# Kernel tuning notes

Measured on AMD Instinct MI355X. Metric: run time of the kernel, lower is better.

## Reference

```python
import jax, jax.numpy as jnp
import numpy as np

N = 100000
E = 1600000
IN = 256
H = 4
C = 64


def setup_inputs() -> dict:
    key = jax.random.key(0)
    k1, k2, k3, k4, k5, k6 = jax.random.split(key, 6)
    x = jax.random.normal(k1, (N, IN), dtype=jnp.float32)
    edge_index = jax.random.randint(k2, (2, E), 0, N, dtype=jnp.int64)
    W = jax.random.normal(k3, (IN, H * C), dtype=jnp.float32) * (1.0 / np.sqrt(IN))
    att_src = jax.random.normal(k4, (H, C), dtype=jnp.float32) * 0.1
    att_dst = jax.random.normal(k5, (H, C), dtype=jnp.float32) * 0.1
    bias = jax.random.normal(k6, (H * C,), dtype=jnp.float32) * 0.01
    return {"x": x, "edge_index": edge_index, "W": W, "att_src": att_src, "att_dst": att_dst, "bias": bias}


def reference(x, edge_index, W, att_src, att_dst, bias):
    n = x.shape[0]
    # PyG GATConv default: add self-loops
    loops = jnp.arange(n, dtype=edge_index.dtype)
    src = jnp.concatenate([edge_index[0], loops])  # [E+N]
    dst = jnp.concatenate([edge_index[1], loops])  # [E+N]
    xp = (x @ W).reshape(n, H, C)                   # [N,H,C]
    a_src = jnp.einsum('nhc,hc->nh', xp, att_src)   # [N,H]
    a_dst = jnp.einsum('nhc,hc->nh', xp, att_dst)   # [N,H]
    # per-edge attention logits, LeakyReLU(0.2)
    alpha = jax.nn.leaky_relu(a_src[src] + a_dst[dst], negative_slope=0.2)  # [E+N,H]
    # segment softmax over destination neighborhoods (every node has a self-loop)
    amax = jax.ops.segment_max(alpha, dst, num_segments=n)
    amax = jnp.where(jnp.isfinite(amax), amax, 0.0)
    ex = jnp.exp(alpha - amax[dst])
    denom = jax.ops.segment_sum(ex, dst, num_segments=n)
    w = ex / denom[dst]                              # [E+N,H]
    # weighted scatter-add of source features
    msg = xp[src] * w[..., None]                     # [E+N,H,C]
    agg = jax.ops.segment_sum(msg, dst, num_segments=n)  # [N,H,C]
    out = agg.reshape(n, H * C) + bias
    return jax.nn.elu(out)
```

## Files before the change

### kernel.cpp

```cpp
#include <hip/hip_runtime.h>
#include <hip/hip_fp16.h>

#define FDIM 256
#define NH 4

typedef float f32x4 __attribute__((ext_vector_type(4)));
typedef int   i32x4 __attribute__((ext_vector_type(4)));
typedef short short8v __attribute__((ext_vector_type(8)));
typedef unsigned short ushort_t;
typedef unsigned short ushort8 __attribute__((ext_vector_type(8)));

__device__ __forceinline__ float leaky02(float v) { return v > 0.0f ? v : 0.2f * v; }

__device__ __forceinline__ ushort_t f2bf(float f) {
    union { float f; unsigned int u; } v; v.f = f;
    unsigned int u = v.u + 0x7FFFu + ((v.u >> 16) & 1u);
    return (ushort_t)(u >> 16);
}

__device__ __forceinline__ float bf2f(ushort_t u) {
    union { float f; unsigned int u; } v;
    v.u = ((unsigned int)u) << 16;
    return v.f;
}

__device__ __forceinline__ void gload_lds16(const void* g, void* lds) {
    __builtin_amdgcn_global_load_lds((const __attribute__((address_space(1))) unsigned int*)g,
                                     (__attribute__((address_space(3))) unsigned int*)lds, 16, 0, 0);
}

__device__ __forceinline__ float recw(const i32x4& r, int h) {
    unsigned v = (h < 2) ? (unsigned)r.y : (unsigned)r.z;
    unsigned bits = (h & 1) ? (v >> 16) : (v & 0xFFFFu);
    __half_raw hr; hr.x = (unsigned short)bits;
    return __half2float(*reinterpret_cast<__half*>(&hr));
}

__global__ __launch_bounds__(256) void wprep_kernel(const float* __restrict__ W,
                                                    ushort_t* __restrict__ Wbf) {
    const int k = blockIdx.x;
    const int col = threadIdx.x;
    Wbf[(((size_t)(k >> 3) * 256 + col) << 3) + (k & 7)] = f2bf(W[(size_t)k * 256 + col]);
}

__global__ __launch_bounds__(512) void gemm_xp_kernel(const float* __restrict__ x,
                                                      const ushort_t* __restrict__ Wbf,
                                                      const float* __restrict__ att_s,
                                                      const float* __restrict__ att_d,
                                                      ushort_t* __restrict__ xpb,
                                                      float* __restrict__ a_src,
                                                      float* __restrict__ a_dst, int n,
                                                      const int* __restrict__ dst,
                                                      int* __restrict__ counts, int E) {
    __shared__ ushort_t a_lds[4096];
    __shared__ ushort_t b_lds[8192];
    const int t = threadIdx.x;

    {
        const int per = (E + gridDim.x - 1) / gridDim.x;
        const int lo = blockIdx.x * per;
        const int hi = min(lo + per, E);
        for (int e = lo + t; e < hi; e += 512)
            atomicAdd(&counts[__builtin_nontemporal_load(&dst[e])], 1);
    }

    const int w = t >> 6, l = t & 63;
    const int wm = w >> 2, wn = w & 3;
    const int row0 = blockIdx.x << 7;
    const int fr = l & 15, fk = l >> 4;

    const int arow = t & 127, akb = t >> 7;
    int grow = row0 + arow;
    if (grow >= n) grow = n - 1;
    const float* aptr = x + (size_t)grow * FDIM + (akb << 3);

    f32x4 acc[4][4] = {};

    for (int s = 0; s < 8; ++s) {
        float4 v0 = *(const float4*)(aptr + s * 32);
        float4 v1 = *(const float4*)(aptr + s * 32 + 4);
        ushort8 u;
        u[0]=f2bf(v0.x); u[1]=f2bf(v0.y); u[2]=f2bf(v0.z); u[3]=f2bf(v0.w);
        u[4]=f2bf(v1.x); u[5]=f2bf(v1.y); u[6]=f2bf(v1.z); u[7]=f2bf(v1.w);

        if (s) __syncthreads();

        *(ushort8*)&a_lds[(((size_t)akb << 7) + arow) << 3] = u;
        gload_lds16(Wbf + (size_t)s * 8192 + ((size_t)t << 3), (char*)b_lds + (w << 10));
        gload_lds16(Wbf + (size_t)s * 8192 + ((size_t)(t + 512) << 3), (char*)b_lds + 8192 + (w << 10));
        __syncthreads();

        short8v af[4], bfv[4];
        #pragma unroll
        for (int m = 0; m < 4; ++m)
            af[m] = *(const short8v*)&a_lds[(((size_t)fk << 7) + wm * 64 + m * 16 + fr) << 3];
        #pragma unroll
        for (int nf = 0; nf < 4; ++nf)
            bfv[nf] = *(const short8v*)&b_lds[(((size_t)fk << 8) + wn * 64 + nf * 16 + fr) << 3];
        #pragma unroll
        for (int m = 0; m < 4; ++m)
            #pragma unroll
            for (int nf = 0; nf < 4; ++nf)
                acc[m][nf] = __builtin_amdgcn_mfma_f32_16x16x32_bf16(af[m], bfv[nf], acc[m][nf], 0, 0, 0);
    }

    #pragma unroll
    for (int m = 0; m < 4; ++m) {
        const int r_ = row0 + wm * 64 + m * 16 + fk * 4;
        #pragma unroll
        for (int nf = 0; nf < 4; ++nf) {
            const int c_ = wn * 64 + nf * 16 + fr;
            #pragma unroll
            for (int j = 0; j < 4; ++j)
                if (r_ + j < n)
                    xpb[(size_t)(r_ + j) * FDIM + c_] = f2bf(acc[m][nf][j]);
        }
    }

    float att_sv[4], att_dv[4];
    #pragma unroll
    for (int nf = 0; nf < 4; ++nf) {
        att_sv[nf] = att_s[(wn << 6) + (nf << 4) + fr];
        att_dv[nf] = att_d[(wn << 6) + (nf << 4) + fr];
    }
    #pragma unroll
    for (int m = 0; m < 4; ++m) {
        #pragma unroll
        for (int j = 0; j < 4; ++j) {
            float ps = acc[m][0][j] * att_sv[0] + acc[m][1][j] * att_sv[1]
                     + acc[m][2][j] * att_sv[2] + acc[m][3][j] * att_sv[3];
            float pd = acc[m][0][j] * att_dv[0] + acc[m][1][j] * att_dv[1]
                     + acc[m][2][j] * att_dv[2] + acc[m][3][j] * att_dv[3];
            ps += __shfl_xor(ps, 1, 64); pd += __shfl_xor(pd, 1, 64);
            ps += __shfl_xor(ps, 2, 64); pd += __shfl_xor(pd, 2, 64);
            ps += __shfl_xor(ps, 4, 64); pd += __shfl_xor(pd, 4, 64);
            ps += __shfl_xor(ps, 8, 64); pd += __shfl_xor(pd, 8, 64);
            if (fr == 0) {
                const int r_ = row0 + wm * 64 + m * 16 + fk * 4 + j;
                if (r_ < n) {
                    a_src[r_ * NH + wn] = ps;
                    a_dst[r_ * NH + wn] = pd;
                }
            }
        }
    }
}

__global__ __launch_bounds__(256) void scan_partial_kernel(const int* __restrict__ counts,
                                                           int* __restrict__ blockSums, int n) {
    __shared__ int sdata[256];
    const int b = blockIdx.x, t = threadIdx.x;
    const int base = b * 1024 + t * 4;
    int s = 0;
    #pragma unroll
    for (int j = 0; j < 4; ++j)
        if (base + j < n) s += counts[base + j];
    sdata[t] = s;
    __syncthreads();
    for (int off = 128; off > 0; off >>= 1) {
        if (t < off) sdata[t] += sdata[t + off];
        __syncthreads();
    }
    if (t == 0) blockSums[b] = sdata[0];
}

__global__ __launch_bounds__(256) void scan_final_kernel(const int* __restrict__ counts,
                                                         const int* __restrict__ blockSums,
                                                         int* __restrict__ offsets,
                                                         int* __restrict__ cursor, int n, int nb) {
    __shared__ int s[256];
    __shared__ int bs[256];
    const int b = blockIdx.x, t = threadIdx.x;
    int bv = (t < nb) ? blockSums[t] : 0;
    bs[t] = bv;
    __syncthreads();
    for (int d = 1; d < 256; d <<= 1) {
        int u = (t >= d) ? bs[t - d] : 0;
        __syncthreads();
        bs[t] += u;
        __syncthreads();
    }
    const int blockOff = (b > 0) ? bs[b - 1] : 0;

    const int base = b * 1024 + t * 4;
    int c[4];
    int tsum = 0;
    #pragma unroll
    for (int j = 0; j < 4; ++j) {
        c[j] = (base + j < n) ? counts[base + j] : 0;
        tsum += c[j];
    }
    s[t] = tsum;
    __syncthreads();
    for (int d = 1; d < 256; d <<= 1) {
        int u = (t >= d) ? s[t - d] : 0;
        __syncthreads();
        s[t] += u;
        __syncthreads();
    }
    int run = s[t] - tsum + blockOff;
    #pragma unroll
    for (int j = 0; j < 4; ++j) {
        if (base + j < n) {
            offsets[base + j] = run;
            cursor[base + j] = run;
            run += c[j];
        }
    }
}

__global__ void scatter_kernel(const int* __restrict__ src, const int* __restrict__ dst,
                               const float* __restrict__ a_src, const float* __restrict__ a_dst,
                               int* __restrict__ cursor, i32x4* __restrict__ erec, int E) {
    int stride = gridDim.x * blockDim.x;
    for (int e = blockIdx.x * blockDim.x + threadIdx.x; e < E; e += stride) {
        const int s = __builtin_nontemporal_load(&src[e]);
        const int d = __builtin_nontemporal_load(&dst[e]);
        const float4 as = ((const float4*)a_src)[s];
        const float4 ad = ((const float4*)a_dst)[d];
        const float w0 = __expf(leaky02(as.x + ad.x));
        const float w1 = __expf(leaky02(as.y + ad.y));
        const float w2 = __expf(leaky02(as.z + ad.z));
        const float w3 = __expf(leaky02(as.w + ad.w));
        union { __half2 h; int i; } p01, p23;
        p01.h = __floats2half2_rn(w0, w1);
        p23.h = __floats2half2_rn(w2, w3);
        i32x4 rec;
        rec.x = s; rec.y = p01.i; rec.z = p23.i; rec.w = 0;
        const int pos = atomicAdd(&cursor[d], 1);
        __builtin_nontemporal_store(rec, &erec[pos]);
    }
}

__global__ __launch_bounds__(256) void aggregate_kernel(const ushort_t* __restrict__ xpb,
                                                        const float* __restrict__ a_src,
                                                        const float* __restrict__ a_dst,
                                                        const int* __restrict__ offsets,
                                                        const int* __restrict__ counts,
                                                        const i32x4* __restrict__ erec,
                                                        const float* __restrict__ bias,
                                                        float* __restrict__ out, int n) {
    const int i = (blockIdx.x << 2) + (threadIdx.x >> 6);
    if (i >= n) return;
    const int lane = threadIdx.x & 63;
    const int halfid = lane >> 5, sl = lane & 31;
    const int h = sl >> 3;
    const size_t colb = (size_t)sl << 3;
    const int start = offsets[i];
    const int cnt = counts[i];
    const i32x4* recs = erec + start;

    float acc[8] = {};
    float den = 0.f;

    int e = 0;
    for (; e + 8 <= cnt; e += 8) {
        const i32x4* rp = recs + e + (halfid << 2);
        const i32x4 r0 = rp[0];
        const i32x4 r1 = rp[1];
        const i32x4 r2 = rp[2];
        const i32x4 r3 = rp[3];
        const ushort8 u0 = *(const ushort8*)(xpb + (size_t)r0.x * FDIM + colb);
        const ushort8 u1 = *(const ushort8*)(xpb + (size_t)r1.x * FDIM + colb);
        const ushort8 u2 = *(const ushort8*)(xpb + (size_t)r2.x * FDIM + colb);
        const ushort8 u3 = *(const ushort8*)(xpb + (size_t)r3.x * FDIM + colb);
        const float w0 = recw(r0, h), w1 = recw(r1, h), w2 = recw(r2, h), w3 = recw(r3, h);
        den += (w0 + w1) + (w2 + w3);
        #pragma unroll
        for (int j = 0; j < 8; ++j) acc[j] = fmaf(w0, bf2f(u0[j]), acc[j]);
        #pragma unroll
        for (int j = 0; j < 8; ++j) acc[j] = fmaf(w1, bf2f(u1[j]), acc[j]);
        #pragma unroll
        for (int j = 0; j < 8; ++j) acc[j] = fmaf(w2, bf2f(u2[j]), acc[j]);
        #pragma unroll
        for (int j = 0; j < 8; ++j) acc[j] = fmaf(w3, bf2f(u3[j]), acc[j]);
    }
    for (; e + 2 <= cnt; e += 2) {
        const i32x4 r = recs[e + halfid];
        const ushort8 u = *(const ushort8*)(xpb + (size_t)r.x * FDIM + colb);
        const float wv = recw(r, h);
        den += wv;
        #pragma unroll
        for (int j = 0; j < 8; ++j) acc[j] = fmaf(wv, bf2f(u[j]), acc[j]);
    }
    {
        int srcidx;
        float wv;
        if (halfid == 0) {
            srcidx = i;
            wv = __expf(leaky02(a_src[i * NH + h] + a_dst[i * NH + h]));
        } else if (e < cnt) {
            const i32x4 r = recs[e];
            srcidx = r.x;
            wv = recw(r, h);
        } else {
            srcidx = i;
            wv = 0.f;
        }
        const ushort8 u = *(const ushort8*)(xpb + (size_t)srcidx * FDIM + colb);
        den += wv;
        #pragma unroll
        for (int j = 0; j < 8; ++j) acc[j] = fmaf(wv, bf2f(u[j]), acc[j]);
    }
    den += __shfl_xor(den, 32, 64);
    #pragma unroll
    for (int j = 0; j < 8; ++j) acc[j] += __shfl_xor(acc[j], 32, 64);

    const float inv = 1.0f / den;
    const int c0 = (sl << 3) + (halfid << 2);
    const float4 b4 = *(const float4*)(bias + c0);
    const int jb = halfid << 2;
    f32x4 v;
    v.x = acc[jb + 0] * inv + b4.x;
    v.y = acc[jb + 1] * inv + b4.y;
    v.z = acc[jb + 2] * inv + b4.z;
    v.w = acc[jb + 3] * inv + b4.w;
    v.x = v.x > 0.f ? v.x : (__expf(v.x) - 1.f);
    v.y = v.y > 0.f ? v.y : (__expf(v.y) - 1.f);
    v.z = v.z > 0.f ? v.z : (__expf(v.z) - 1.f);
    v.w = v.w > 0.f ? v.w : (__expf(v.w) - 1.f);
    *(f32x4*)(out + (size_t)i * FDIM + c0) = v;
}

extern "C" void kernel_launch(void* const* d_in, const int* in_sizes, int n_in,
                              void* d_out, int out_size, void* d_ws, size_t ws_size,
                              hipStream_t stream) {
    const float* x       = (const float*)d_in[0];
    const int*   ei      = (const int*)d_in[1];
    const float* W       = (const float*)d_in[2];
    const float* att_s   = (const float*)d_in[3];
    const float* att_d   = (const float*)d_in[4];
    const float* bias    = (const float*)d_in[5];
    float* out = (float*)d_out;

    const int n = in_sizes[0] / FDIM;
    const int E = in_sizes[1] / 2;
    const int* src = ei;
    const int* dst = ei + E;

    char* ws = (char*)d_ws;
    size_t off = 0;
    auto alloc = [&](size_t bytes) -> void* {
        void* p = ws + off;
        off = (off + bytes + 255) & ~(size_t)255;
        return p;
    };
    ushort_t* xpb  = (ushort_t*)alloc((size_t)n * FDIM * sizeof(ushort_t));
    float* a_src   = (float*)alloc((size_t)n * NH * sizeof(float));
    float* a_dst   = (float*)alloc((size_t)n * NH * sizeof(float));
    int* counts    = (int*)alloc((size_t)n * sizeof(int));
    int* offsets   = (int*)alloc((size_t)n * sizeof(int));
    int* cursor    = (int*)alloc((size_t)n * sizeof(int));
    int* blockSums = (int*)alloc(256 * sizeof(int));
    i32x4* erec    = (i32x4*)alloc((size_t)E * sizeof(i32x4));
    ushort_t* Wbf  = (ushort_t*)alloc((size_t)FDIM * FDIM * sizeof(ushort_t));
    (void)ws_size;

    hipMemsetAsync(counts, 0, (size_t)n * sizeof(int), stream);

    wprep_kernel<<<256, 256, 0, stream>>>(W, Wbf);
    gemm_xp_kernel<<<(n + 127) / 128, 512, 0, stream>>>(x, Wbf, att_s, att_d, xpb, a_src, a_dst, n,
                                                        dst, counts, E);
    const int nb = (n + 1023) / 1024;
    scan_partial_kernel<<<nb, 256, 0, stream>>>(counts, blockSums, n);
    scan_final_kernel<<<nb, 256, 0, stream>>>(counts, blockSums, offsets, cursor, n, nb);
    scatter_kernel<<<2048, 256, 0, stream>>>(src, dst, a_src, a_dst, cursor, erec, E);
    aggregate_kernel<<<(n + 3) / 4, 256, 0, stream>>>(xpb, a_src, a_dst, offsets, counts, erec, bias, out, n);
}
```

Measured before the change: 341.8 us.

## Store only source indices in CSR and recompute attention weights in aggregate

Result: slower. 390.2 us (+14.2%).

```diff
diff --git a/kernel.cpp b/kernel.cpp
--- a/kernel.cpp
+++ b/kernel.cpp
@@ -27,13 +27,6 @@
 __device__ __forceinline__ void gload_lds16(const void* g, void* lds) {
     __builtin_amdgcn_global_load_lds((const __attribute__((address_space(1))) unsigned int*)g,
                                      (__attribute__((address_space(3))) unsigned int*)lds, 16, 0, 0);
-}
-
-__device__ __forceinline__ float recw(const i32x4& r, int h) {
-    unsigned v = (h < 2) ? (unsigned)r.y : (unsigned)r.z;
-    unsigned bits = (h & 1) ? (v >> 16) : (v & 0xFFFFu);
-    __half_raw hr; hr.x = (unsigned short)bits;
-    return __half2float(*reinterpret_cast<__half*>(&hr));
 }
 
 __global__ __launch_bounds__(256) void wprep_kernel(const float* __restrict__ W,
@@ -209,26 +202,25 @@
     }
 }
 
-__global__ void scatter_kernel(const int* __restrict__ src, const int* __restrict__ dst,
-                               const float* __restrict__ a_src, const float* __restrict__ a_dst,
-                               int* __restrict__ cursor, i32x4* __restrict__ erec, int E) {
-    int stride = gridDim.x * blockDim.x;
-    for (int e = blockIdx.x * blockDim.x + threadIdx.x; e < E; e += stride) {
-        const int s = __builtin_nontemporal_load(&src[e]);
-        const int d = __builtin_nontemporal_load(&dst[e]);
-        const float4 as = ((const float4*)a_src)[s];
-        const float4 ad = ((const float4*)a_dst)[d];
-        const float w0 = __expf(leaky02(as.x + ad.x));
-        const float w1 = __expf(leaky02(as.y + ad.y));
-        const float w2 = __expf(leaky02(as.z + ad.z));
-        const float w3 = __expf(leaky02(as.w + ad.w));
-        union { __half2 h; int i; } p01, p23;
-        p01.h = __floats2half2_rn(w0, w1);
-        p23.h = __floats2half2_rn(w2, w3);
-        i32x4 rec;
-        rec.x = s; rec.y = p01.i; rec.z = p23.i; rec.w = 0;
-        const int pos = atomicAdd(&cursor[d], 1);
-        __builtin_nontemporal_store(rec, &erec[pos]);
+__global__ __launch_bounds__(256) void scatter_kernel(const int* __restrict__ src,
+                                                      const int* __restrict__ dst,
+                                                      int* __restrict__ cursor,
+                                                      int* __restrict__ csr, int E) {
+    const int stride4 = gridDim.x * blockDim.x;
+    const int nq = E >> 2;
+    for (int q = blockIdx.x * blockDim.x + threadIdx.x; q < nq; q += stride4) {
+        const i32x4 s4 = __builtin_nontemporal_load(&((const i32x4*)src)[q]);
+        const i32x4 d4 = __builtin_nontemporal_load(&((const i32x4*)dst)[q]);
+        #pragma unroll
+        for (int j = 0; j < 4; ++j) {
+            const int pos = atomicAdd(&cursor[d4[j]], 1);
+            csr[pos] = s4[j];
+        }
+    }
+    if (blockIdx.x == 0 && threadIdx.x < (E & 3)) {
+        const int e = (nq << 2) + threadIdx.x;
+        const int pos = atomicAdd(&cursor[dst[e]], 1);
+        csr[pos] = src[e];
     }
 }
 
@@ -237,7 +229,7 @@
                                                         const float* __restrict__ a_dst,
                                                         const int* __restrict__ offsets,
                                                         const int* __restrict__ counts,
-                                                        const i32x4* __restrict__ erec,
+                                                        const int* __restrict__ csr,
                                                         const float* __restrict__ bias,
                                                         float* __restrict__ out, int n) {
     const int i = (blockIdx.x << 2) + (threadIdx.x >> 6);
@@ -248,37 +240,30 @@
     const size_t colb = (size_t)sl << 3;
     const int start = offsets[i];
     const int cnt = counts[i];
-    const i32x4* recs = erec + start;
+    const int* csrp = csr + start;
+    const float adv = a_dst[i * NH + h];
 
     float acc[8] = {};
     float den = 0.f;
 
     int e = 0;
-    for (; e + 8 <= cnt; e += 8) {
-        const i32x4* rp = recs + e + (halfid << 2);
-        const i32x4 r0 = rp[0];
-        const i32x4 r1 = rp[1];
-        const i32x4 r2 = rp[2];
-        const i32x4 r3 = rp[3];
-        const ushort8 u0 = *(const ushort8*)(xpb + (size_t)r0.x * FDIM + colb);
-        const ushort8 u1 = *(const ushort8*)(xpb + (size_t)r1.x * FDIM + colb);
-        const ushort8 u2 = *(const ushort8*)(xpb + (size_t)r2.x * FDIM + colb);
-        const ushort8 u3 = *(const ushort8*)(xpb + (size_t)r3.x * FDIM + colb);
-        const float w0 = recw(r0, h), w1 = recw(r1, h), w2 = recw(r2, h), w3 = recw(r3, h);
-        den += (w0 + w1) + (w2 + w3);
-        #pragma unroll
-        for (int j = 0; j < 8; ++j) acc[j] = fmaf(w0, bf2f(u0[j]), acc[j]);
-        #pragma unroll
-        for (int j = 0; j < 8; ++j) acc[j] = fmaf(w1, bf2f(u1[j]), acc[j]);
-        #pragma unroll
-        for (int j = 0; j < 8; ++j) acc[j] = fmaf(w2, bf2f(u2[j]), acc[j]);
-        #pragma unroll
-        for (int j = 0; j < 8; ++j) acc[j] = fmaf(w3, bf2f(u3[j]), acc[j]);
+    for (; e + 4 <= cnt; e += 4) {
+        const int sa = csrp[e + halfid];
+        const int sb = csrp[e + 2 + halfid];
+        const ushort8 ua = *(const ushort8*)(xpb + (size_t)sa * FDIM + colb);
+        const ushort8 ub = *(const ushort8*)(xpb + (size_t)sb * FDIM + colb);
+        const float wa = __expf(leaky02(a_src[sa * NH + h] + adv));
+        const float wb = __expf(leaky02(a_src[sb * NH + h] + adv));
+        den += wa + wb;
+        #pragma unroll
+        for (int j = 0; j < 8; ++j) acc[j] = fmaf(wa, bf2f(ua[j]), acc[j]);
+        #pragma unroll
+        for (int j = 0; j < 8; ++j) acc[j] = fmaf(wb, bf2f(ub[j]), acc[j]);
     }
     for (; e + 2 <= cnt; e += 2) {
-        const i32x4 r = recs[e + halfid];
-        const ushort8 u = *(const ushort8*)(xpb + (size_t)r.x * FDIM + colb);
-        const float wv = recw(r, h);
+        const int s = csrp[e + halfid];
+        const ushort8 u = *(const ushort8*)(xpb + (size_t)s * FDIM + colb);
+        const float wv = __expf(leaky02(a_src[s * NH + h] + adv));
         den += wv;
         #pragma unroll
         for (int j = 0; j < 8; ++j) acc[j] = fmaf(wv, bf2f(u[j]), acc[j]);
@@ -288,11 +273,10 @@
         float wv;
         if (halfid == 0) {
             srcidx = i;
-            wv = __expf(leaky02(a_src[i * NH + h] + a_dst[i * NH + h]));
+            wv = __expf(leaky02(a_src[i * NH + h] + adv));
         } else if (e < cnt) {
-            const i32x4 r = recs[e];
-            srcidx = r.x;
-            wv = recw(r, h);
+            srcidx = csrp[e];
+            wv = __expf(leaky02(a_src[srcidx * NH + h] + adv));
         } else {
             srcidx = i;
             wv = 0.f;
@@ -352,7 +336,7 @@
     int* offsets   = (int*)alloc((size_t)n * sizeof(int));
     int* cursor    = (int*)alloc((size_t)n * sizeof(int));
     int* blockSums = (int*)alloc(256 * sizeof(int));
-    i32x4* erec    = (i32x4*)alloc((size_t)E * sizeof(i32x4));
+    int* csr       = (int*)alloc((size_t)E * sizeof(int));
     ushort_t* Wbf  = (ushort_t*)alloc((size_t)FDIM * FDIM * sizeof(ushort_t));
     (void)ws_size;
 
@@ -364,6 +348,6 @@
     const int nb = (n + 1023) / 1024;
     scan_partial_kernel<<<nb, 256, 0, stream>>>(counts, blockSums, n);
     scan_final_kernel<<<nb, 256, 0, stream>>>(counts, blockSums, offsets, cursor, n, nb);
-    scatter_kernel<<<2048, 256, 0, stream>>>(src, dst, a_src, a_dst, cursor, erec, E);
-    aggregate_kernel<<<(n + 3) / 4, 256, 0, stream>>>(xpb, a_src, a_dst, offsets, counts, erec, bias, out, n);
-}
+    scatter_kernel<<<2048, 256, 0, stream>>>(src, dst, cursor, csr, E);
+    aggregate_kernel<<<(n + 3) / 4, 256, 0, stream>>>(xpb, a_src, a_dst, offsets, counts, csr, bias, out, n);
+}
```
